# Performance work log

Measured on AMD Instinct MI355X. Metric: run time of the kernel, lower is better.

## Reference

```python
import jax, jax.numpy as jnp
import numpy as np

TOP_K = 2
NORM_P = 1  # moe_normalize_expert_weights


def setup_inputs() -> dict:
    key = jax.random.key(0)
    k1, k2 = jax.random.split(key)
    B, S, H, E = 4, 4096, 4096, 64
    x = jax.random.normal(k1, (B, S, H), dtype=jnp.float32)
    # Linear(H, E, bias=False) weight, torch layout [E, H]
    W = jax.random.normal(k2, (E, H), dtype=jnp.float32) * (1.0 / np.sqrt(H))
    return {"x": x, "W": W}


def reference(x, W):
    H = x.shape[-1]
    xt = x.reshape(-1, H)                      # [T, H]
    logits = jnp.einsum('th,eh->te', xt, W)    # [T, E]
    scores = jax.nn.softmax(logits, axis=-1)   # [T, E]
    expert_weights, expert_indices = jax.lax.top_k(scores, TOP_K)  # [T, K]
    # p=1 norm over the selected weights (values are positive post-softmax)
    norm = jnp.sum(jnp.abs(expert_weights), axis=-1, keepdims=True)
    expert_weights = expert_weights / norm
    return scores, expert_weights, expert_indices
```

## Files before the change

kernel.cpp:

```cpp
#include <hip/hip_runtime.h>
#include <math.h>

#define TOKS  16384
#define HD    4096
#define NE    64
#define MT    32
#define KT    64
#define NTHR  256
#define LST   72
#define NTILE (HD / KT)

typedef unsigned int   u32;
typedef unsigned short u16;
typedef short v8s __attribute__((ext_vector_type(8)));
typedef float v4f __attribute__((ext_vector_type(4)));

__device__ __forceinline__ void split2(float a, float b, u32& hi, u32& lo) {
    u32 ua = __float_as_uint(a), ub = __float_as_uint(b);
    hi = (ub & 0xffff0000u) | (ua >> 16);
    float la = a - __uint_as_float(ua & 0xffff0000u);
    float lb = b - __uint_as_float(ub & 0xffff0000u);
    lo = (__float_as_uint(lb) & 0xffff0000u) | (__float_as_uint(la) >> 16);
}

__global__ __launch_bounds__(256) void wsplit_kernel(const float* __restrict__ W,
                                                     u16* __restrict__ wh, u16* __restrict__ wl) {
    const int gid = blockIdx.x * 256 + threadIdx.x;
    const float4 f = ((const float4*)W)[gid];
    u32 h0, h1, l0, l1;
    split2(f.x, f.y, h0, l0);
    split2(f.z, f.w, h1, l1);
    u32* whp = (u32*)wh; u32* wlp = (u32*)wl;
    whp[gid * 2 + 0] = h0; whp[gid * 2 + 1] = h1;
    wlp[gid * 2 + 0] = l0; wlp[gid * 2 + 1] = l1;
}

__global__ __launch_bounds__(NTHR, 2) void router_kernel(
    const float* __restrict__ x, const u16* __restrict__ wh, const u16* __restrict__ wl,
    float* __restrict__ scores, float* __restrict__ wout, float* __restrict__ iout)
{
    __shared__ u16 Xh[2][MT][LST], Xl[2][MT][LST];
    __shared__ u16 Wh[2][NE][LST], Wl[2][NE][LST];
    __shared__ float Ls[MT][NE + 1];
    __shared__ float Ssum[MT], Smax[MT];

    const int t    = threadIdx.x;
    const int tok0 = blockIdx.x * MT;
    const int srow = t >> 3, sc = t & 7;
    const int wrow = t >> 2, wc = t & 3;
    const int lane = t & 63;
    const int w    = t >> 6;
    const int wt   = w & 1;
    const int weh  = w >> 1;
    const int q    = lane >> 4, r = lane & 15;
    const int arow  = wt * 16 + r;
    const int brow0 = weh * 32 + r;
    const int brow1 = weh * 32 + 16 + r;

    v4f acc0 = {0.f, 0.f, 0.f, 0.f};
    v4f acc1 = {0.f, 0.f, 0.f, 0.f};

    const size_t xbase = (size_t)(tok0 + srow) * HD;
    const size_t wbase = (size_t)wrow * HD;

    float4 xr0, xr1;
    uint4  whr0, whr1, wlr0, wlr1;

#define LOAD_TILE(K0)                                               \
    do {                                                            \
        xr0  = *(const float4*)&x[xbase + (K0) + sc * 4];           \
        xr1  = *(const float4*)&x[xbase + (K0) + 32 + sc * 4];      \
        whr0 = *(const uint4*)&wh[wbase + (K0) + wc * 8];           \
        whr1 = *(const uint4*)&wh[wbase + (K0) + 32 + wc * 8];      \
        wlr0 = *(const uint4*)&wl[wbase + (K0) + wc * 8];           \
        wlr1 = *(const uint4*)&wl[wbase + (K0) + 32 + wc * 8];      \
    } while (0)

#define STORE_TILE(B)                                               \
    do {                                                            \
        u32 h0, h1, l0, l1;                                         \
        split2(xr0.x, xr0.y, h0, l0);                               \
        split2(xr0.z, xr0.w, h1, l1);                               \
        *(uint2*)&Xh[B][srow][sc * 4]      = make_uint2(h0, h1);    \
        *(uint2*)&Xl[B][srow][sc * 4]      = make_uint2(l0, l1);    \
        split2(xr1.x, xr1.y, h0, l0);                               \
        split2(xr1.z, xr1.w, h1, l1);                               \
        *(uint2*)&Xh[B][srow][32 + sc * 4] = make_uint2(h0, h1);    \
        *(uint2*)&Xl[B][srow][32 + sc * 4] = make_uint2(l0, l1);    \
        *(uint4*)&Wh[B][wrow][wc * 8]      = whr0;                  \
        *(uint4*)&Wh[B][wrow][32 + wc * 8] = whr1;                  \
        *(uint4*)&Wl[B][wrow][wc * 8]      = wlr0;                  \
        *(uint4*)&Wl[B][wrow][32 + wc * 8] = wlr1;                  \
    } while (0)

    LOAD_TILE(0);
    STORE_TILE(0);
    __syncthreads();

    for (int tile = 0; tile < NTILE; ++tile) {
        const int buf = tile & 1;
        if (tile + 1 < NTILE) LOAD_TILE((tile + 1) * KT);
#pragma unroll
        for (int c = 0; c < 2; ++c) {
            const int ko = c * 32 + q * 8;
            v8s ah  = *(const v8s*)&Xh[buf][arow][ko];
            v8s al  = *(const v8s*)&Xl[buf][arow][ko];
            v8s bh0 = *(const v8s*)&Wh[buf][brow0][ko];
            v8s bl0 = *(const v8s*)&Wl[buf][brow0][ko];
            v8s bh1 = *(const v8s*)&Wh[buf][brow1][ko];
            v8s bl1 = *(const v8s*)&Wl[buf][brow1][ko];
            acc0 = __builtin_amdgcn_mfma_f32_16x16x32_bf16(ah, bh0, acc0, 0, 0, 0);
            acc0 = __builtin_amdgcn_mfma_f32_16x16x32_bf16(al, bh0, acc0, 0, 0, 0);
            acc0 = __builtin_amdgcn_mfma_f32_16x16x32_bf16(ah, bl0, acc0, 0, 0, 0);
            acc1 = __builtin_amdgcn_mfma_f32_16x16x32_bf16(ah, bh1, acc1, 0, 0, 0);
            acc1 = __builtin_amdgcn_mfma_f32_16x16x32_bf16(al, bh1, acc1, 0, 0, 0);
            acc1 = __builtin_amdgcn_mfma_f32_16x16x32_bf16(ah, bl1, acc1, 0, 0, 0);
        }
        if (tile + 1 < NTILE) STORE_TILE(buf ^ 1);
        __syncthreads();
    }

#pragma unroll
    for (int reg = 0; reg < 4; ++reg) {
        Ls[wt * 16 + q * 4 + reg][weh * 32 + r]      = acc0[reg];
        Ls[wt * 16 + q * 4 + reg][weh * 32 + 16 + r] = acc1[reg];
    }
    __syncthreads();

    if (t < MT) {
        const int tk = t;
        float m = -3.402823466e+38f;
        for (int e = 0; e < NE; ++e) m = fmaxf(m, Ls[tk][e]);
        float s = 0.f;
        float v1 = -1.f, v2 = -1.f;
        int   i1 = 0, i2 = 0;
        for (int e = 0; e < NE; ++e) {
            const float ex = expf(Ls[tk][e] - m);
            s += ex;
            if (ex > v1)      { v2 = v1; i2 = i1; v1 = ex; i1 = e; }
            else if (ex > v2) { v2 = ex; i2 = e; }
        }
        const float s1 = v1 / s, s2 = v2 / s;
        const float ws_ = s1 + s2;
        wout[(size_t)(tok0 + tk) * 2 + 0] = s1 / ws_;
        wout[(size_t)(tok0 + tk) * 2 + 1] = s2 / ws_;
        iout[(size_t)(tok0 + tk) * 2 + 0] = (float)i1;
        iout[(size_t)(tok0 + tk) * 2 + 1] = (float)i2;
        Ssum[tk] = s;
        Smax[tk] = m;
    }
    __syncthreads();

#pragma unroll
    for (int it = 0; it < (MT * NE) / NTHR; ++it) {
        const int f  = it * NTHR + t;
        const int tk = f >> 6, e = f & 63;
        scores[(size_t)(tok0 + tk) * NE + e] = expf(Ls[tk][e] - Smax[tk]) / Ssum[tk];
    }
}

extern "C" void kernel_launch(void* const* d_in, const int* in_sizes, int n_in,
                              void* d_out, int out_size, void* d_ws, size_t ws_size,
                              hipStream_t stream) {
    (void)in_sizes; (void)n_in; (void)out_size; (void)ws_size;
    const float* x = (const float*)d_in[0];
    const float* W = (const float*)d_in[1];
    float* out    = (float*)d_out;
    float* scores = out;
    float* wout   = scores + (size_t)TOKS * NE;
    float* iout   = wout   + (size_t)TOKS * 2;

    u16* wh = (u16*)d_ws;
    u16* wl = wh + (size_t)NE * HD;

    wsplit_kernel<<<dim3(256), dim3(256), 0, stream>>>(W, wh, wl);
    router_kernel<<<dim3(TOKS / MT), dim3(NTHR), 0, stream>>>(x, wh, wl, scores, wout, iout);
}
```

Before: 392.5 us.

## Feed MFMA operands straight from global memory, dropping LDS staging and barriers

Removes the shared-memory double buffer and the per-tile __syncthreads. Each lane now loads its MFMA fragment of x and of the split W directly from global memory into registers, and the bf16 hi/lo split is done in registers. The token tile is halved to 16 and the occupancy hint raised to 4 blocks per CU, so each of the four waves computes one 16x16 expert slice. The aim is to cut LDS traffic and synchronisation. In exchange, global loads become strided per lane rather than row-coalesced, and each x element is re-split by all four waves.

```diff
diff --git a/kernel.cpp b/kernel.cpp
--- a/kernel.cpp
+++ b/kernel.cpp
@@ -4,10 +4,9 @@
 #define TOKS  16384
 #define HD    4096
 #define NE    64
-#define MT    32
+#define MT    16
 #define KT    64
 #define NTHR  256
-#define LST   72
 #define NTILE (HD / KT)
 
 typedef unsigned int   u32;
@@ -35,96 +34,75 @@
     wlp[gid * 2 + 0] = l0; wlp[gid * 2 + 1] = l1;
 }
 
-__global__ __launch_bounds__(NTHR, 2) void router_kernel(
+union U4S8 { uint4 u; v8s s; };
+
+__global__ __launch_bounds__(NTHR, 4) void router_kernel(
     const float* __restrict__ x, const u16* __restrict__ wh, const u16* __restrict__ wl,
     float* __restrict__ scores, float* __restrict__ wout, float* __restrict__ iout)
 {
-    __shared__ u16 Xh[2][MT][LST], Xl[2][MT][LST];
-    __shared__ u16 Wh[2][NE][LST], Wl[2][NE][LST];
     __shared__ float Ls[MT][NE + 1];
     __shared__ float Ssum[MT], Smax[MT];
 
     const int t    = threadIdx.x;
     const int tok0 = blockIdx.x * MT;
-    const int srow = t >> 3, sc = t & 7;
-    const int wrow = t >> 2, wc = t & 3;
     const int lane = t & 63;
     const int w    = t >> 6;
-    const int wt   = w & 1;
-    const int weh  = w >> 1;
-    const int q    = lane >> 4, r = lane & 15;
-    const int arow  = wt * 16 + r;
-    const int brow0 = weh * 32 + r;
-    const int brow1 = weh * 32 + 16 + r;
+    const int q    = lane >> 4;
+    const int r    = lane & 15;
 
-    v4f acc0 = {0.f, 0.f, 0.f, 0.f};
-    v4f acc1 = {0.f, 0.f, 0.f, 0.f};
+    const size_t xrow = (size_t)(tok0 + r) * HD;
+    const size_t wrow = (size_t)(w * 16 + r) * HD;
+    const int q8 = q * 8;
 
-    const size_t xbase = (size_t)(tok0 + srow) * HD;
-    const size_t wbase = (size_t)wrow * HD;
+    v4f acc = {0.f, 0.f, 0.f, 0.f};
 
-    float4 xr0, xr1;
-    uint4  whr0, whr1, wlr0, wlr1;
+    float4 ax[2][4];
+    uint4  bw[2][4];
 
-#define LOAD_TILE(K0)                                               \
-    do {                                                            \
-        xr0  = *(const float4*)&x[xbase + (K0) + sc * 4];           \
-        xr1  = *(const float4*)&x[xbase + (K0) + 32 + sc * 4];      \
-        whr0 = *(const uint4*)&wh[wbase + (K0) + wc * 8];           \
-        whr1 = *(const uint4*)&wh[wbase + (K0) + 32 + wc * 8];      \
-        wlr0 = *(const uint4*)&wl[wbase + (K0) + wc * 8];           \
-        wlr1 = *(const uint4*)&wl[wbase + (K0) + 32 + wc * 8];      \
+#define LOADT(S, K0)                                                   \
+    do {                                                               \
+        ax[S][0] = *(const float4*)&x[xrow + (K0) + q8];               \
+        ax[S][1] = *(const float4*)&x[xrow + (K0) + q8 + 4];           \
+        ax[S][2] = *(const float4*)&x[xrow + (K0) + 32 + q8];          \
+        ax[S][3] = *(const float4*)&x[xrow + (K0) + 32 + q8 + 4];      \
+        bw[S][0] = *(const uint4*)&wh[wrow + (K0) + q8];               \
+        bw[S][1] = *(const uint4*)&wh[wrow + (K0) + 32 + q8];          \
+        bw[S][2] = *(const uint4*)&wl[wrow + (K0) + q8];               \
+        bw[S][3] = *(const uint4*)&wl[wrow + (K0) + 32 + q8];          \
     } while (0)
 
-#define STORE_TILE(B)                                               \
-    do {                                                            \
-        u32 h0, h1, l0, l1;                                         \
-        split2(xr0.x, xr0.y, h0, l0);                               \
-        split2(xr0.z, xr0.w, h1, l1);                               \
-        *(uint2*)&Xh[B][srow][sc * 4]      = make_uint2(h0, h1);    \
-        *(uint2*)&Xl[B][srow][sc * 4]      = make_uint2(l0, l1);    \
-        split2(xr1.x, xr1.y, h0, l0);                               \
-        split2(xr1.z, xr1.w, h1, l1);                               \
-        *(uint2*)&Xh[B][srow][32 + sc * 4] = make_uint2(h0, h1);    \
-        *(uint2*)&Xl[B][srow][32 + sc * 4] = make_uint2(l0, l1);    \
-        *(uint4*)&Wh[B][wrow][wc * 8]      = whr0;                  \
-        *(uint4*)&Wh[B][wrow][32 + wc * 8] = whr1;                  \
-        *(uint4*)&Wl[B][wrow][wc * 8]      = wlr0;                  \
-        *(uint4*)&Wl[B][wrow][32 + wc * 8] = wlr1;                  \
+#define COMPUTE(S)                                                     \
+    do {                                                               \
+        _Pragma("unroll")                                              \
+        for (int c = 0; c < 2; ++c) {                                  \
+            const float4 p = ax[S][2 * c], s2 = ax[S][2 * c + 1];      \
+            u32 h0, l0, h1, l1, h2, l2, h3, l3;                        \
+            split2(p.x, p.y, h0, l0);  split2(p.z, p.w, h1, l1);       \
+            split2(s2.x, s2.y, h2, l2); split2(s2.z, s2.w, h3, l3);    \
+            U4S8 ah, al, bh, bl;                                       \
+            ah.u = make_uint4(h0, h1, h2, h3);                         \
+            al.u = make_uint4(l0, l1, l2, l3);                         \
+            bh.u = bw[S][c];                                           \
+            bl.u = bw[S][2 + c];                                       \
+            acc = __builtin_amdgcn_mfma_f32_16x16x32_bf16(ah.s, bh.s, acc, 0, 0, 0); \
+            acc = __builtin_amdgcn_mfma_f32_16x16x32_bf16(al.s, bh.s, acc, 0, 0, 0); \
+            acc = __builtin_amdgcn_mfma_f32_16x16x32_bf16(ah.s, bl.s, acc, 0, 0, 0); \
+        }                                                              \
     } while (0)
 
-    LOAD_TILE(0);
-    STORE_TILE(0);
-    __syncthreads();
-
+    LOADT(0, 0);
+#pragma unroll 2
     for (int tile = 0; tile < NTILE; ++tile) {
         const int buf = tile & 1;
-        if (tile + 1 < NTILE) LOAD_TILE((tile + 1) * KT);
-#pragma unroll
-        for (int c = 0; c < 2; ++c) {
-            const int ko = c * 32 + q * 8;
-            v8s ah  = *(const v8s*)&Xh[buf][arow][ko];
-            v8s al  = *(const v8s*)&Xl[buf][arow][ko];
-            v8s bh0 = *(const v8s*)&Wh[buf][brow0][ko];
-            v8s bl0 = *(const v8s*)&Wl[buf][brow0][ko];
-            v8s bh1 = *(const v8s*)&Wh[buf][brow1][ko];
-            v8s bl1 = *(const v8s*)&Wl[buf][brow1][ko];
-            acc0 = __builtin_amdgcn_mfma_f32_16x16x32_bf16(ah, bh0, acc0, 0, 0, 0);
-            acc0 = __builtin_amdgcn_mfma_f32_16x16x32_bf16(al, bh0, acc0, 0, 0, 0);
-            acc0 = __builtin_amdgcn_mfma_f32_16x16x32_bf16(ah, bl0, acc0, 0, 0, 0);
-            acc1 = __builtin_amdgcn_mfma_f32_16x16x32_bf16(ah, bh1, acc1, 0, 0, 0);
-            acc1 = __builtin_amdgcn_mfma_f32_16x16x32_bf16(al, bh1, acc1, 0, 0, 0);
-            acc1 = __builtin_amdgcn_mfma_f32_16x16x32_bf16(ah, bl1, acc1, 0, 0, 0);
-        }
-        if (tile + 1 < NTILE) STORE_TILE(buf ^ 1);
-        __syncthreads();
+        if (tile + 1 < NTILE) LOADT(buf ^ 1, (tile + 1) * KT);
+        COMPUTE(buf);
     }
+#undef LOADT
+#undef COMPUTE
 
 #pragma unroll
-    for (int reg = 0; reg < 4; ++reg) {
-        Ls[wt * 16 + q * 4 + reg][weh * 32 + r]      = acc0[reg];
-        Ls[wt * 16 + q * 4 + reg][weh * 32 + 16 + r] = acc1[reg];
-    }
+    for (int reg = 0; reg < 4; ++reg)
+        Ls[q * 4 + reg][w * 16 + r] = acc[reg];
     __syncthreads();
 
     if (t < MT) {
```

Result: slower. 504.9 us (+28.6%).
